# Optimization experiments

Hardware: AMD Instinct MI355X
Metric: run time of the kernel (lower is better)

## Reference

```python
import jax, jax.numpy as jnp
import numpy as np

D_MODEL = 1024
N_HEADS = 16
DEPTH = D_MODEL // N_HEADS
B, S = 2, 2048


def setup_inputs() -> dict:
    key = jax.random.key(0)
    ks = jax.random.split(key, 11)
    scale = 1.0 / np.sqrt(D_MODEL)
    return {
        "q": jax.random.normal(ks[0], (B, S, D_MODEL), jnp.float32),
        "k": jax.random.normal(ks[1], (B, S, D_MODEL), jnp.float32),
        "v": jax.random.normal(ks[2], (B, S, D_MODEL), jnp.float32),
        "wq": jax.random.normal(ks[3], (D_MODEL, D_MODEL), jnp.float32) * scale,
        "bq": jnp.zeros((D_MODEL,), jnp.float32),
        "wk": jax.random.normal(ks[4], (D_MODEL, D_MODEL), jnp.float32) * scale,
        "bk": jnp.zeros((D_MODEL,), jnp.float32),
        "wv": jax.random.normal(ks[5], (D_MODEL, D_MODEL), jnp.float32) * scale,
        "bv": jnp.zeros((D_MODEL,), jnp.float32),
        "wo": jax.random.normal(ks[6], (D_MODEL, D_MODEL), jnp.float32) * scale,
        "bo": jnp.zeros((D_MODEL,), jnp.float32),
    }


def _mha(q, k, v, wq, bq, wk, bk, wv, bv, wo, bo):
    b, s, _ = q.shape
    # separate QKV projections
    qh = (q @ wq + bq).reshape(b, s, N_HEADS, DEPTH).transpose(0, 2, 1, 3)  # [b,h,s,d]
    kh = (k @ wk + bk).reshape(b, s, N_HEADS, DEPTH).transpose(0, 2, 1, 3)
    vh = (v @ wv + bv).reshape(b, s, N_HEADS, DEPTH).transpose(0, 2, 1, 3)
    # keras.layers.Attention default: UNSCALED dot-product scores, causal mask
    scores = jnp.einsum("bhqd,bhkd->bhqk", qh, kh)  # [b,h,s,s]
    causal = jnp.tril(jnp.ones((s, s), bool))
    scores = jnp.where(causal, scores, jnp.float32(-1e9))
    attn = jax.nn.softmax(scores, axis=-1)
    out = jnp.einsum("bhqk,bhkd->bhqd", attn, vh)  # [b,h,s,d]
    out = out.transpose(0, 2, 1, 3).reshape(b, s, D_MODEL)
    return out @ wo + bo


def reference(q, k, v, wq, bq, wk, bk, wv, bv, wo, bo):
    return _mha(q, k, v, wq, bq, wk, bk, wv, bv, wo, bo)
```

## Files before the change

kernel.cpp:

```cpp
#include <hip/hip_runtime.h>
#include <stdint.h>

#define AS1q __attribute__((address_space(1)))
#define AS3q __attribute__((address_space(3)))

typedef unsigned short US;
typedef __bf16 bf16x8 __attribute__((ext_vector_type(8)));
typedef float f32x4 __attribute__((ext_vector_type(4)));
typedef float f32x16 __attribute__((ext_vector_type(16)));
typedef float f32x2 __attribute__((ext_vector_type(2)));
typedef __bf16 bf16x2 __attribute__((ext_vector_type(2)));

#define LOG2E 1.44269504088896340736f

__device__ __forceinline__ US f2bf(float f) {
  union { float f; uint32_t u; } c; c.f = f;
  uint32_t u = c.u;
  return (US)((u + 0x7fffu + ((u >> 16) & 1u)) >> 16);
}

__device__ __forceinline__ bf16x8 asb(uint4 u) {
  union { uint4 u; bf16x8 b; } c; c.u = u; return c.b;
}

__device__ __forceinline__ uint32_t pk2(float a, float b) {
  f32x2 fv; fv[0] = a; fv[1] = b;
  bf16x2 bb = __builtin_convertvector(fv, bf16x2);
  union { bf16x2 b; uint32_t u; } c; c.b = bb; return c.u;
}

__device__ __forceinline__ void gload16(const void* g, void* l) {
  __builtin_amdgcn_global_load_lds((AS1q void*)(void*)g, (AS3q void*)l, 16, 0, 0);
}

__global__ void prep_kernel(const float* __restrict__ q, const float* __restrict__ k,
                            const float* __restrict__ v,
                            const float* __restrict__ w0, const float* __restrict__ w1,
                            const float* __restrict__ w2, const float* __restrict__ w3,
                            US* __restrict__ qb, US* __restrict__ kb, US* __restrict__ vb,
                            US* __restrict__ t0, US* __restrict__ t1,
                            US* __restrict__ t2, US* __restrict__ t3) {
  __shared__ US T[64 * 68];
  const int bx = blockIdx.x;
  const int t = threadIdx.x;
  if (bx < 6144) {
    const int ten = bx >> 11, chunk = bx & 2047;
    const float* s; US* d;
    if (ten == 0)      { s = q; d = qb; }
    else if (ten == 1) { s = k; d = kb; }
    else               { s = v; d = vb; }
    int i = (chunk * 256 + t) * 8;
    float4 f0 = *(const float4*)&s[i];
    float4 f1 = *(const float4*)&s[i + 4];
    ushort4 u0, u1;
    u0.x = f2bf(f0.x); u0.y = f2bf(f0.y); u0.z = f2bf(f0.z); u0.w = f2bf(f0.w);
    u1.x = f2bf(f1.x); u1.y = f2bf(f1.y); u1.z = f2bf(f1.z); u1.w = f2bf(f1.w);
    *(ushort4*)&d[i] = u0;
    *(ushort4*)&d[i + 4] = u1;
    return;
  }
  const int idx = bx - 6144;
  const int wsel = idx >> 8, rem = idx & 255;
  const int n0 = (rem & 15) * 64, k0 = (rem >> 4) * 64;
  const float* W; US* Wt;
  if (wsel == 0)      { W = w0; Wt = t0; }
  else if (wsel == 1) { W = w1; Wt = t1; }
  else if (wsel == 2) { W = w2; Wt = t2; }
  else                { W = w3; Wt = t3; }
#pragma unroll
  for (int it = 0; it < 4; ++it) {
    int p = t + it * 256;
    int row = p >> 4, c4 = (p & 15) * 4;
    float4 f = *(const float4*)&W[(k0 + row) * 1024 + n0 + c4];
    ushort4 u;
    u.x = f2bf(f.x); u.y = f2bf(f.y); u.z = f2bf(f.z); u.w = f2bf(f.w);
    *(ushort4*)&T[row * 68 + c4] = u;
  }
  __syncthreads();
#pragma unroll
  for (int it = 0; it < 4; ++it) {
    int p = t + it * 256;
    int rn = p >> 4, ck = (p & 15) * 4;
    ushort4 o;
    o.x = T[(ck + 0) * 68 + rn];
    o.y = T[(ck + 1) * 68 + rn];
    o.z = T[(ck + 2) * 68 + rn];
    o.w = T[(ck + 3) * 68 + rn];
    *(ushort4*)&Wt[(n0 + rn) * 1024 + k0 + ck] = o;
  }
}

template <bool SWAP>
__device__ __forceinline__ void gemm_core(const US* A, const US* Wt,
                                          int m0, int n0, US* As, US* Bs,
                                          f32x4 acc[4][4]) {
  const int tid = threadIdx.x;
  const int wave = tid >> 6, lane = tid & 63;
  const int quad = lane >> 4, l16 = lane & 15;
  const int wm = wave >> 1, wn = wave & 1;
#pragma unroll
  for (int i = 0; i < 4; ++i)
#pragma unroll
    for (int j = 0; j < 4; ++j) acc[i][j] = (f32x4)0.0f;
  const int p = wave * 64 + lane;
  const int arow0 = p >> 2, koff = (p & 3) * 8;
  for (int k0 = 0; k0 < 1024; k0 += 32) {
    gload16(A + (m0 + arow0) * 1024 + k0 + koff, As + wave * 512);
    gload16(A + (m0 + arow0 + 64) * 1024 + k0 + koff, As + 2048 + wave * 512);
    gload16(Wt + (n0 + arow0) * 1024 + k0 + koff, Bs + wave * 512);
    gload16(Wt + (n0 + arow0 + 64) * 1024 + k0 + koff, Bs + 2048 + wave * 512);
    __syncthreads();
    uint4 af[4], bf_[4];
#pragma unroll
    for (int mt = 0; mt < 4; ++mt)
      af[mt] = *(const uint4*)&As[(wm * 64 + mt * 16 + l16) * 32 + quad * 8];
#pragma unroll
    for (int nt = 0; nt < 4; ++nt)
      bf_[nt] = *(const uint4*)&Bs[(wn * 64 + nt * 16 + l16) * 32 + quad * 8];
#pragma unroll
    for (int i = 0; i < 4; ++i)
#pragma unroll
      for (int j = 0; j < 4; ++j) {
        if (SWAP)
          acc[i][j] = __builtin_amdgcn_mfma_f32_16x16x32_bf16(asb(bf_[i]), asb(af[j]),
                                                              acc[i][j], 0, 0, 0);
        else
          acc[i][j] = __builtin_amdgcn_mfma_f32_16x16x32_bf16(asb(af[i]), asb(bf_[j]),
                                                              acc[i][j], 0, 0, 0);
      }
    __syncthreads();
  }
}

__global__ __launch_bounds__(256, 4) void gemm_qkv_kernel(
    const US* __restrict__ qb, const US* __restrict__ kb, const US* __restrict__ vb,
    const US* __restrict__ wfT,
    const float* __restrict__ bq, const float* __restrict__ bk, const float* __restrict__ bv,
    US* __restrict__ qh, US* __restrict__ kh, US* __restrict__ vt) {
  __shared__ __align__(16) US As[4096], Bs[4096];
  const int m0 = blockIdx.x * 128, n0 = blockIdx.y * 128;
  const int which = n0 >> 10;
  const int nl0 = n0 & 1023;
  const US* A = (which == 0) ? qb : (which == 1) ? kb : vb;
  const float* bias = (which == 0) ? bq : (which == 1) ? bk : bv;
  const int tid = threadIdx.x, wave = tid >> 6, lane = tid & 63;
  const int quad = lane >> 4, l16 = lane & 15;
  const int wm = wave >> 1, wn = wave & 1;
  f32x4 acc[4][4];
  if (which == 2) {
    gemm_core<true>(A, wfT, m0, n0, As, Bs, acc);
#pragma unroll
    for (int nt = 0; nt < 4; ++nt) {
      int dg = nl0 + wn * 64 + nt * 16 + quad * 4;
#pragma unroll
      for (int r = 0; r < 4; ++r) {
        int d = dg + r;
        float bval = bias[d];
        int hh = d >> 6, dd = d & 63;
#pragma unroll
        for (int mt = 0; mt < 4; ++mt) {
          int sg = m0 + wm * 64 + mt * 16;
          int bb = sg >> 11, ss = sg & 2047;
          vt[(((size_t)bb * 16 + hh) * 64 + dd) * 2048 + ss + l16] =
              f2bf(acc[nt][mt][r] + bval);
        }
      }
    }
  } else {
    gemm_core<false>(A, wfT, m0, n0, As, Bs, acc);
    US* O = (which == 0) ? qh : kh;
    const float scale = (which == 0) ? LOG2E : 1.0f;
#pragma unroll
    for (int nt = 0; nt < 4; ++nt) {
      int nl = nl0 + wn * 64 + nt * 16 + l16;
      float bval = bias[nl];
      int hh = nl >> 6, d = nl & 63;
#pragma unroll
      for (int mt = 0; mt < 4; ++mt) {
#pragma unroll
        for (int r = 0; r < 4; ++r) {
          int m = m0 + wm * 64 + mt * 16 + quad * 4 + r;
          int bb = m >> 11, s = m & 2047;
          O[((bb * 16 + hh) * 2048 + s) * 64 + d] = f2bf((acc[mt][nt][r] + bval) * scale);
        }
      }
    }
  }
}

__global__ __launch_bounds__(256, 4) void gemm_out_kernel(
    const US* __restrict__ ao, const US* __restrict__ woT,
    const float* __restrict__ bo, float* __restrict__ out) {
  __shared__ __align__(16) US As[4096], Bs[2048];
  const int m0 = blockIdx.x * 128, n0 = blockIdx.y * 64;
  const int tid = threadIdx.x;
  const int wave = tid >> 6, lane = tid & 63;
  const int quad = lane >> 4, l16 = lane & 15;
  f32x4 acc[2][4];
#pragma unroll
  for (int i = 0; i < 2; ++i)
#pragma unroll
    for (int j = 0; j < 4; ++j) acc[i][j] = (f32x4)0.0f;
  const int arow0 = tid >> 2, koff = (tid & 3) * 8;
  for (int k0 = 0; k0 < 1024; k0 += 32) {
    gload16(ao + (m0 + arow0) * 1024 + k0 + koff, As + wave * 512);
    gload16(ao + (m0 + arow0 + 64) * 1024 + k0 + koff, As + 2048 + wave * 512);
    gload16(woT + (n0 + arow0) * 1024 + k0 + koff, Bs + wave * 512);
    __syncthreads();
    uint4 af[2], bf_[4];
#pragma unroll
    for (int mt = 0; mt < 2; ++mt)
      af[mt] = *(const uint4*)&As[(wave * 32 + mt * 16 + l16) * 32 + quad * 8];
#pragma unroll
    for (int nt = 0; nt < 4; ++nt)
      bf_[nt] = *(const uint4*)&Bs[(nt * 16 + l16) * 32 + quad * 8];
#pragma unroll
    for (int mt = 0; mt < 2; ++mt)
#pragma unroll
      for (int nt = 0; nt < 4; ++nt)
        acc[mt][nt] = __builtin_amdgcn_mfma_f32_16x16x32_bf16(asb(af[mt]), asb(bf_[nt]),
                                                              acc[mt][nt], 0, 0, 0);
    __syncthreads();
  }
#pragma unroll
  for (int nt = 0; nt < 4; ++nt) {
    int n = n0 + nt * 16 + l16;
    float bval = bo[n];
#pragma unroll
    for (int mt = 0; mt < 2; ++mt) {
#pragma unroll
      for (int r = 0; r < 4; ++r) {
        int m = m0 + wave * 32 + mt * 16 + quad * 4 + r;
        out[m * 1024 + n] = acc[mt][nt][r] + bval;
      }
    }
  }
}

__global__ __launch_bounds__(256, 2) void attn_kernel(
    const US* __restrict__ qh, const US* __restrict__ kh,
    const US* __restrict__ vt, US* __restrict__ aout) {
  __shared__ __align__(16) char arena[73728];
  US* KsA = (US*)arena;
  US* VsA = (US*)(arena + 32768);
  US* Qs  = (US*)(arena + 65536);
  float* Oex = (float*)arena;
  float* lEx = (float*)(arena + 34816);

  const int tid = threadIdx.x;
  const int wave = tid >> 6, lane = tid & 63;
  const int l31 = lane & 31, lh = lane >> 5;
  const int w_m = wave & 1, w_k = wave >> 1;
  const int bh = blockIdx.x;
  const int b = bh >> 4, h = bh & 15;
  const int jg = blockIdx.y;

  const US* gkb = kh + (size_t)bh * 2048 * 64;
  const US* gvb = vt + (size_t)bh * 64 * 2048;

  for (int ei = 0; ei < 2; ++ei) {
    const int qt = ei ? jg : (31 - jg);
    const int q0 = qt * 64;
    const int nit = (qt >> 1) + 1;
    __syncthreads();
    {
      const US* gq = qh + ((size_t)bh * 2048 + q0) * 64;
#pragma unroll
      for (int ro = 0; ro < 2; ++ro) {
        int p = tid + ro * 256;
        int row = p >> 3, c = (p & 7) ^ (row & 7);
        gload16(gq + row * 64 + c * 8, Qs + ro * 2048 + wave * 512);
      }
#pragma unroll
      for (int ro = 0; ro < 4; ++ro) {
        int p = tid + ro * 256;
        int row = p >> 3, c = (p & 7) ^ (row & 7);
        gload16(gkb + row * 64 + c * 8, KsA + ro * 2048 + wave * 512);
      }
#pragma unroll
      for (int ro = 0; ro < 4; ++ro) {
        int p = tid + ro * 256;
        int row = p >> 4, c = (p & 15) ^ (row & 15);
        gload16(gvb + row * 2048 + c * 8, VsA + ro * 2048 + wave * 512);
      }
    }
    __syncthreads();

    const int qrow = w_m * 32 + l31;
    uint4 bq[4];
#pragma unroll
    for (int s = 0; s < 4; ++s)
      bq[s] = *(const uint4*)&Qs[qrow * 64 + (((2 * s + lh) ^ (qrow & 7)) * 8)];
    const int q_g = q0 + qrow;

    float l_lane = 0.0f;
    f32x16 Oa0 = (f32x16)0.0f, Oa1 = (f32x16)0.0f;

    for (int it = 0; it < nit; ++it) {
      const int cb = it & 1;
      const int kb = it * 128;
      if (it) __syncthreads();
      if (it + 1 < nit) {
        const US* gk = gkb + (kb + 128) * 64;
        const US* gv = gvb + (kb + 128);
        US* kd = KsA + (cb ^ 1) * 8192;
        US* vd = VsA + (cb ^ 1) * 8192;
#pragma unroll
        for (int ro = 0; ro < 4; ++ro) {
          int p = tid + ro * 256;
          int row = p >> 3, c = (p & 7) ^ (row & 7);
          gload16(gk + row * 64 + c * 8, kd + ro * 2048 + wave * 512);
        }
#pragma unroll
        for (int ro = 0; ro < 4; ++ro) {
          int p = tid + ro * 256;
          int row = p >> 4, c = (p & 15) ^ (row & 15);
          gload16(gv + row * 2048 + c * 8, vd + ro * 2048 + wave * 512);
        }
      }
      const US* Kc = KsA + cb * 8192;
      const US* Vc = VsA + cb * 8192;

      f32x16 sa0 = (f32x16)0.0f, sa1 = (f32x16)0.0f;
#pragma unroll
      for (int s = 0; s < 4; ++s) {
        int kr0 = w_k * 64 + l31;
        uint4 ka0 = *(const uint4*)&Kc[kr0 * 64 + (((2 * s + lh) ^ (kr0 & 7)) * 8)];
        sa0 = __builtin_amdgcn_mfma_f32_32x32x16_bf16(asb(ka0), asb(bq[s]), sa0, 0, 0, 0);
      }
#pragma unroll
      for (int s = 0; s < 4; ++s) {
        int kr1 = w_k * 64 + 32 + l31;
        uint4 ka1 = *(const uint4*)&Kc[kr1 * 64 + (((2 * s + lh) ^ (kr1 & 7)) * 8)];
        sa1 = __builtin_amdgcn_mfma_f32_32x32x16_bf16(asb(ka1), asb(bq[s]), sa1, 0, 0, 0);
      }

      const bool diag = (it == nit - 1);
      float e[2][16];
#pragma unroll
      for (int ta = 0; ta < 2; ++ta) {
        const int kbase = kb + w_k * 64 + ta * 32 + 4 * lh;
#pragma unroll
        for (int r = 0; r < 16; ++r) {
          float sv = ta ? sa1[r] : sa0[r];
          float ev = __builtin_amdgcn_exp2f(sv);
          if (diag) {
            int key_g = kbase + (r & 3) + 8 * (r >> 2);
            if (key_g > q_g) ev = 0.0f;
          }
          e[ta][r] = ev;
          l_lane += ev;
        }
      }

#pragma unroll
      for (int ta = 0; ta < 2; ++ta) {
#pragma unroll
        for (int s2 = 0; s2 < 2; ++s2) {
          uint32_t PA0 = pk2(e[ta][8 * s2 + 0], e[ta][8 * s2 + 1]);
          uint32_t PA1 = pk2(e[ta][8 * s2 + 2], e[ta][8 * s2 + 3]);
          uint32_t PB0 = pk2(e[ta][8 * s2 + 4], e[ta][8 * s2 + 5]);
          uint32_t PB1 = pk2(e[ta][8 * s2 + 6], e[ta][8 * s2 + 7]);
          uint32_t XA0 = (uint32_t)__shfl_xor((int)PA0, 32, 64);
          uint32_t XA1 = (uint32_t)__shfl_xor((int)PA1, 32, 64);
          uint32_t XB0 = (uint32_t)__shfl_xor((int)PB0, 32, 64);
          uint32_t XB1 = (uint32_t)__shfl_xor((int)PB1, 32, 64);
          uint4 bp;
          bp.x = lh ? XB0 : PA0;
          bp.y = lh ? XB1 : PA1;
          bp.z = lh ? PB0 : XA0;
          bp.w = lh ? PB1 : XA1;
          const int c_log = w_k * 8 + ta * 4 + s2 * 2 + lh;
          int vr0 = l31;
          uint4 va0 = *(const uint4*)&Vc[vr0 * 128 + ((c_log ^ (vr0 & 15)) * 8)];
          Oa0 = __builtin_amdgcn_mfma_f32_32x32x16_bf16(asb(va0), asb(bp), Oa0, 0, 0, 0);
          int vr1 = 32 + l31;
          uint4 va1 = *(const uint4*)&Vc[vr1 * 128 + ((c_log ^ (vr1 & 15)) * 8)];
          Oa1 = __builtin_amdgcn_mfma_f32_32x32x16_bf16(asb(va1), asb(bp), Oa1, 0, 0, 0);
        }
      }
    }

    float l_q = l_lane + __shfl_xor(l_lane, 32, 64);

    __syncthreads();
    {
      float* myO = Oex + w_k * (64 * 68);
      int q_idx = w_m * 32 + l31;
#pragma unroll
      for (int r = 0; r < 16; ++r) {
        int dr = 4 * lh + (r & 3) + 8 * (r >> 2);
        myO[q_idx * 68 + dr] = Oa0[r];
        myO[q_idx * 68 + 32 + dr] = Oa1[r];
      }
      if (lh == 0) lEx[w_k * 64 + q_idx] = l_q;
    }
    __syncthreads();
    {
      int q_idx = tid >> 2;
      int dseg = (tid & 3) * 16;
      float inv = 1.0f / (lEx[q_idx] + lEx[64 + q_idx]);
      union { US s[16]; uint4 v[2]; } ob;
#pragma unroll
      for (int t2 = 0; t2 < 16; ++t2) {
        float o = Oex[q_idx * 68 + dseg + t2] + Oex[64 * 68 + q_idx * 68 + dseg + t2];
        ob.s[t2] = f2bf(o * inv);
      }
      US* dst = aout + ((size_t)b * 2048 + q0 + q_idx) * 1024 + h * 64 + dseg;
      *(uint4*)dst = ob.v[0];
      *(uint4*)(dst + 8) = ob.v[1];
    }
  }
}

extern "C" void kernel_launch(void* const* d_in, const int* in_sizes, int n_in,
                              void* d_out, int out_size, void* d_ws, size_t ws_size,
                              hipStream_t stream) {
  const float* q  = (const float*)d_in[0];
  const float* k  = (const float*)d_in[1];
  const float* v  = (const float*)d_in[2];
  const float* wq = (const float*)d_in[3];
  const float* bq = (const float*)d_in[4];
  const float* wk = (const float*)d_in[5];
  const float* bk = (const float*)d_in[6];
  const float* wv = (const float*)d_in[7];
  const float* bv = (const float*)d_in[8];
  const float* wo = (const float*)d_in[9];
  const float* bo = (const float*)d_in[10];
  float* out = (float*)d_out;

  char* ws = (char*)d_ws;
  const size_t MB = 1024 * 1024;
  US* qb  = (US*)(ws + 0 * MB);
  US* kb  = (US*)(ws + 8 * MB);
  US* vb  = (US*)(ws + 16 * MB);
  US* wqT = (US*)(ws + 24 * MB);
  US* wkT = (US*)(ws + 26 * MB);
  US* wvT = (US*)(ws + 28 * MB);
  US* woT = (US*)(ws + 30 * MB);
  US* qh  = (US*)(ws + 32 * MB);
  US* kh  = (US*)(ws + 40 * MB);
  US* vt  = (US*)(ws + 48 * MB);
  US* ao  = (US*)(ws + 56 * MB);

  prep_kernel<<<7168, 256, 0, stream>>>(q, k, v, wq, wk, wv, wo,
                                        qb, kb, vb, wqT, wkT, wvT, woT);
  gemm_qkv_kernel<<<dim3(32, 24), 256, 0, stream>>>(qb, kb, vb, wqT,
                                                    bq, bk, bv, qh, kh, vt);
  attn_kernel<<<dim3(32, 16), 256, 0, stream>>>(qh, kh, vt, ao);
  gemm_out_kernel<<<dim3(32, 16), 256, 0, stream>>>(ao, woT, bo, out);
}
```

Measured before the change: 210.8 us.

## Split attention key tile across 8 waves instead of 4

Doubles the attention block to 512 threads so each of four key-groups of waves handles 32 keys per 128-key tile instead of 64, halving per-wave QK and PV work per iteration. Partial O and row sums are now reduced across four wave groups in shared memory at the end of each query tile. This raises per-block parallelism and latency hiding, at the cost of more reduction traffic, larger launch bounds pressure on registers, and possibly fewer resident blocks given the 72KB LDS arena.

```diff
diff --git a/kernel.cpp b/kernel.cpp
--- a/kernel.cpp
+++ b/kernel.cpp
@@ -237,7 +237,7 @@
   }
 }
 
-__global__ __launch_bounds__(256, 2) void attn_kernel(
+__global__ __launch_bounds__(512, 4) void attn_kernel(
     const US* __restrict__ qh, const US* __restrict__ kh,
     const US* __restrict__ vt, US* __restrict__ aout) {
   __shared__ __align__(16) char arena[73728];
@@ -245,7 +245,7 @@
   US* VsA = (US*)(arena + 32768);
   US* Qs  = (US*)(arena + 65536);
   float* Oex = (float*)arena;
-  float* lEx = (float*)(arena + 34816);
+  float* lEx = (float*)(arena + 69632);
 
   const int tid = threadIdx.x;
   const int wave = tid >> 6, lane = tid & 63;
@@ -265,23 +265,22 @@
     __syncthreads();
     {
       const US* gq = qh + ((size_t)bh * 2048 + q0) * 64;
+      {
+        int p = tid;
+        int row = p >> 3, c = (p & 7) ^ (row & 7);
+        gload16(gq + row * 64 + c * 8, Qs + wave * 512);
+      }
 #pragma unroll
       for (int ro = 0; ro < 2; ++ro) {
-        int p = tid + ro * 256;
+        int p = tid + ro * 512;
         int row = p >> 3, c = (p & 7) ^ (row & 7);
-        gload16(gq + row * 64 + c * 8, Qs + ro * 2048 + wave * 512);
-      }
-#pragma unroll
-      for (int ro = 0; ro < 4; ++ro) {
-        int p = tid + ro * 256;
-        int row = p >> 3, c = (p & 7) ^ (row & 7);
-        gload16(gkb + row * 64 + c * 8, KsA + ro * 2048 + wave * 512);
-      }
-#pragma unroll
-      for (int ro = 0; ro < 4; ++ro) {
-        int p = tid + ro * 256;
+        gload16(gkb + row * 64 + c * 8, KsA + ro * 4096 + wave * 512);
+      }
+#pragma unroll
+      for (int ro = 0; ro < 2; ++ro) {
+        int p = tid + ro * 512;
         int row = p >> 4, c = (p & 15) ^ (row & 15);
-        gload16(gvb + row * 2048 + c * 8, VsA + ro * 2048 + wave * 512);
+        gload16(gvb + row * 2048 + c * 8, VsA + ro * 4096 + wave * 512);
       }
     }
     __syncthreads();
@@ -306,78 +305,65 @@
         US* kd = KsA + (cb ^ 1) * 8192;
         US* vd = VsA + (cb ^ 1) * 8192;
 #pragma unroll
-        for (int ro = 0; ro < 4; ++ro) {
-          int p = tid + ro * 256;
+        for (int ro = 0; ro < 2; ++ro) {
+          int p = tid + ro * 512;
           int row = p >> 3, c = (p & 7) ^ (row & 7);
-          gload16(gk + row * 64 + c * 8, kd + ro * 2048 + wave * 512);
+          gload16(gk + row * 64 + c * 8, kd + ro * 4096 + wave * 512);
         }
 #pragma unroll
-        for (int ro = 0; ro < 4; ++ro) {
-          int p = tid + ro * 256;
+        for (int ro = 0; ro < 2; ++ro) {
+          int p = tid + ro * 512;
           int row = p >> 4, c = (p & 15) ^ (row & 15);
-          gload16(gv + row * 2048 + c * 8, vd + ro * 2048 + wave * 512);
+          gload16(gv + row * 2048 + c * 8, vd + ro * 4096 + wave * 512);
         }
       }
       const US* Kc = KsA + cb * 8192;
       const US* Vc = VsA + cb * 8192;
 
-      f32x16 sa0 = (f32x16)0.0f, sa1 = (f32x16)0.0f;
+      f32x16 sa0 = (f32x16)0.0f;
+      const int kr0 = w_k * 32 + l31;
 #pragma unroll
       for (int s = 0; s < 4; ++s) {
-        int kr0 = w_k * 64 + l31;
         uint4 ka0 = *(const uint4*)&Kc[kr0 * 64 + (((2 * s + lh) ^ (kr0 & 7)) * 8)];
         sa0 = __builtin_amdgcn_mfma_f32_32x32x16_bf16(asb(ka0), asb(bq[s]), sa0, 0, 0, 0);
       }
-#pragma unroll
-      for (int s = 0; s < 4; ++s) {
-        int kr1 = w_k * 64 + 32 + l31;
-        uint4 ka1 = *(const uint4*)&Kc[kr1 * 64 + (((2 * s + lh) ^ (kr1 & 7)) * 8)];
-        sa1 = __builtin_amdgcn_mfma_f32_32x32x16_bf16(asb(ka1), asb(bq[s]), sa1, 0, 0, 0);
-      }
 
       const bool diag = (it == nit - 1);
-      float e[2][16];
-#pragma unroll
-      for (int ta = 0; ta < 2; ++ta) {
-        const int kbase = kb + w_k * 64 + ta * 32 + 4 * lh;
-#pragma unroll
-        for (int r = 0; r < 16; ++r) {
-          float sv = ta ? sa1[r] : sa0[r];
-          float ev = __builtin_amdgcn_exp2f(sv);
-          if (diag) {
-            int key_g = kbase + (r & 3) + 8 * (r >> 2);
-            if (key_g > q_g) ev = 0.0f;
-          }
-          e[ta][r] = ev;
-          l_lane += ev;
+      float e[16];
+      const int kbase = kb + w_k * 32 + 4 * lh;
+#pragma unroll
+      for (int r = 0; r < 16; ++r) {
+        float ev = __builtin_amdgcn_exp2f(sa0[r]);
+        if (diag) {
+          int key_g = kbase + (r & 3) + 8 * (r >> 2);
+          if (key_g > q_g) ev = 0.0f;
         }
-      }
-
-#pragma unroll
-      for (int ta = 0; ta < 2; ++ta) {
-#pragma unroll
-        for (int s2 = 0; s2 < 2; ++s2) {
-          uint32_t PA0 = pk2(e[ta][8 * s2 + 0], e[ta][8 * s2 + 1]);
-          uint32_t PA1 = pk2(e[ta][8 * s2 + 2], e[ta][8 * s2 + 3]);
-          uint32_t PB0 = pk2(e[ta][8 * s2 + 4], e[ta][8 * s2 + 5]);
-          uint32_t PB1 = pk2(e[ta][8 * s2 + 6], e[ta][8 * s2 + 7]);
-          uint32_t XA0 = (uint32_t)__shfl_xor((int)PA0, 32, 64);
-          uint32_t XA1 = (uint32_t)__shfl_xor((int)PA1, 32, 64);
-          uint32_t XB0 = (uint32_t)__shfl_xor((int)PB0, 32, 64);
-          uint32_t XB1 = (uint32_t)__shfl_xor((int)PB1, 32, 64);
-          uint4 bp;
-          bp.x = lh ? XB0 : PA0;
-          bp.y = lh ? XB1 : PA1;
-          bp.z = lh ? PB0 : XA0;
-          bp.w = lh ? PB1 : XA1;
-          const int c_log = w_k * 8 + ta * 4 + s2 * 2 + lh;
-          int vr0 = l31;
-          uint4 va0 = *(const uint4*)&Vc[vr0 * 128 + ((c_log ^ (vr0 & 15)) * 8)];
-          Oa0 = __builtin_amdgcn_mfma_f32_32x32x16_bf16(asb(va0), asb(bp), Oa0, 0, 0, 0);
-          int vr1 = 32 + l31;
-          uint4 va1 = *(const uint4*)&Vc[vr1 * 128 + ((c_log ^ (vr1 & 15)) * 8)];
-          Oa1 = __builtin_amdgcn_mfma_f32_32x32x16_bf16(asb(va1), asb(bp), Oa1, 0, 0, 0);
-        }
+        e[r] = ev;
+        l_lane += ev;
+      }
+
+#pragma unroll
+      for (int s2 = 0; s2 < 2; ++s2) {
+        uint32_t PA0 = pk2(e[8 * s2 + 0], e[8 * s2 + 1]);
+        uint32_t PA1 = pk2(e[8 * s2 + 2], e[8 * s2 + 3]);
+        uint32_t PB0 = pk2(e[8 * s2 + 4], e[8 * s2 + 5]);
+        uint32_t PB1 = pk2(e[8 * s2 + 6], e[8 * s2 + 7]);
+        uint32_t XA0 = (uint32_t)__shfl_xor((int)PA0, 32, 64);
+        uint32_t XA1 = (uint32_t)__shfl_xor((int)PA1, 32, 64);
+        uint32_t XB0 = (uint32_t)__shfl_xor((int)PB0, 32, 64);
+        uint32_t XB1 = (uint32_t)__shfl_xor((int)PB1, 32, 64);
+        uint4 bp;
+        bp.x = lh ? XB0 : PA0;
+        bp.y = lh ? XB1 : PA1;
+        bp.z = lh ? PB0 : XA0;
+        bp.w = lh ? PB1 : XA1;
+        const int c_log = w_k * 4 + s2 * 2 + lh;
+        int vr0 = l31;
+        uint4 va0 = *(const uint4*)&Vc[vr0 * 128 + ((c_log ^ (vr0 & 15)) * 8)];
+        Oa0 = __builtin_amdgcn_mfma_f32_32x32x16_bf16(asb(va0), asb(bp), Oa0, 0, 0, 0);
+        int vr1 = 32 + l31;
+        uint4 va1 = *(const uint4*)&Vc[vr1 * 128 + ((c_log ^ (vr1 & 15)) * 8)];
+        Oa1 = __builtin_amdgcn_mfma_f32_32x32x16_bf16(asb(va1), asb(bp), Oa1, 0, 0, 0);
       }
     }
 
@@ -397,18 +383,20 @@
     }
     __syncthreads();
     {
-      int q_idx = tid >> 2;
-      int dseg = (tid & 3) * 16;
-      float inv = 1.0f / (lEx[q_idx] + lEx[64 + q_idx]);
-      union { US s[16]; uint4 v[2]; } ob;
-#pragma unroll
-      for (int t2 = 0; t2 < 16; ++t2) {
-        float o = Oex[q_idx * 68 + dseg + t2] + Oex[64 * 68 + q_idx * 68 + dseg + t2];
+      int q_idx = tid >> 3;
+      int dseg = (tid & 7) * 8;
+      float inv = 1.0f / (lEx[q_idx] + lEx[64 + q_idx] + lEx[128 + q_idx] + lEx[192 + q_idx]);
+      union { US s[8]; uint4 v; } ob;
+#pragma unroll
+      for (int t2 = 0; t2 < 8; ++t2) {
+        float o = Oex[q_idx * 68 + dseg + t2]
+                + Oex[64 * 68 + q_idx * 68 + dseg + t2]
+                + Oex[2 * 64 * 68 + q_idx * 68 + dseg + t2]
+                + Oex[3 * 64 * 68 + q_idx * 68 + dseg + t2];
         ob.s[t2] = f2bf(o * inv);
       }
       US* dst = aout + ((size_t)b * 2048 + q0 + q_idx) * 1024 + h * 64 + dseg;
-      *(uint4*)dst = ob.v[0];
-      *(uint4*)(dst + 8) = ob.v[1];
+      *(uint4*)dst = ob.v;
     }
   }
 }
@@ -447,6 +435,6 @@
                                         qb, kb, vb, wqT, wkT, wvT, woT);
   gemm_qkv_kernel<<<dim3(32, 24), 256, 0, stream>>>(qb, kb, vb, wqT,
                                                     bq, bk, bv, qh, kh, vt);
-  attn_kernel<<<dim3(32, 16), 256, 0, stream>>>(qh, kh, vt, ao);
+  attn_kernel<<<dim3(32, 16), 512, 0, stream>>>(qh, kh, vt, ao);
   gemm_out_kernel<<<dim3(32, 16), 256, 0, stream>>>(ao, woT, bo, out);
 }
```

Result: faster. 205.7 us (-2.4%).
